# Kernel tuning notes

Measured on AMD Instinct MI355X. Metric: run time of the kernel, lower is better.

The kernel has to match this reference:

```python
import jax, jax.numpy as jnp
import numpy as np

INPUT_DIM = 1024
OUTPUT_DIM = 1024
DEGREE = 8


def setup_inputs() -> dict:
    key = jax.random.key(0)
    k1, k2 = jax.random.split(key)
    x = jax.random.normal(k1, (8192, INPUT_DIM), dtype=jnp.float32)
    std = 1.0 / (INPUT_DIM * (DEGREE + 1))
    cheby_coeffs = jax.random.normal(k2, (INPUT_DIM, OUTPUT_DIM, DEGREE + 1), dtype=jnp.float32) * std
    return {"x": x, "cheby_coeffs": cheby_coeffs}


def reference(x, cheby_coeffs):
    # x: [B, I]; cheby_coeffs: [I, O, D+1]
    degree = cheby_coeffs.shape[-1] - 1
    t = jnp.clip(jnp.tanh(x), -0.999, 0.999)            # [B, I]
    theta = jnp.arccos(t)[..., None]                     # [B, I, 1]
    arange = jnp.arange(degree + 1, dtype=x.dtype)       # [D+1]
    basis = jnp.cos(theta * arange)                      # [B, I, D+1] Chebyshev T_d(t)
    y = jnp.einsum('bid,iod->bo', basis, cheby_coeffs)   # [B, O]
    return y
```

## Files before the change

### kernel.cpp

```cpp
#include <hip/hip_runtime.h>
#include <stdint.h>

#define B_ROWS 8192
#define I_DIM  1024
#define N_DIM  1024
#define NDEG   9
#define K_DIM  (I_DIM * (NDEG-1))

#define BM 256
#define BN 128
#define BK 64
#define NT (K_DIM / BK)

typedef __attribute__((ext_vector_type(8)))  short short8;
typedef __attribute__((ext_vector_type(16))) float f32x16;

__device__ __forceinline__ unsigned short f2bf(float f) {
  union { float f; uint32_t u; } v; v.f = f;
  uint32_t u = v.u;
  u += 0x7FFFu + ((u >> 16) & 1u);
  return (unsigned short)(u >> 16);
}

__device__ __forceinline__ float bf2f(unsigned short h) {
  union { uint32_t u; float f; } v; v.u = ((uint32_t)h) << 16;
  return v.f;
}

__device__ __forceinline__ uint32_t pk_bf16(float lo, float hi) {
  uint32_t r;
  asm("v_cvt_pk_bf16_f32 %0, %1, %2" : "=v"(r) : "v"(lo), "v"(hi));
  return r;
}

__device__ __forceinline__ float fast_tanh(float x) {
  float e = __expf(2.0f * x);
  return 1.0f - __fdividef(2.0f, e + 1.0f);
}

__device__ __forceinline__ int h2(int r) { return (r >> 2) & 7; }

__global__ __launch_bounds__(256) void repack_kernel(const float* __restrict__ cf,
                                                     unsigned short* __restrict__ Bt,
                                                     float* __restrict__ bias) {
  __shared__ unsigned short L[32][584];
  const int i0  = blockIdx.x * 32;
  const int o0  = blockIdx.y * 64;
  const int tid = threadIdx.x;

  #pragma unroll
  for (int j = 0; j < 18; ++j) {
    const int f4  = j * 256 + tid;
    const int il  = f4 / 144;
    const int odq = f4 % 144;
    const float4 v = *reinterpret_cast<const float4*>(
        cf + ((size_t)(i0 + il) * N_DIM + o0) * NDEG + (size_t)odq * 4);
    ushort4 w;
    w.x = f2bf(v.x); w.y = f2bf(v.y); w.z = f2bf(v.z); w.w = f2bf(v.w);
    *reinterpret_cast<ushort4*>(&L[il][odq * 4]) = w;
  }
  __syncthreads();

  const int o  = tid >> 2;
  const int ci = tid & 3;
  const size_t base = (size_t)(o0 + o) * K_DIM + (size_t)(i0 + ci * 8) * 8;
  #pragma unroll
  for (int p = 0; p < 8; ++p) {
    const int il = ci * 8 + p;
    uint4 u;
    u.x = (uint32_t)L[il][o*9 + 1] | ((uint32_t)L[il][o*9 + 2] << 16);
    u.y = (uint32_t)L[il][o*9 + 3] | ((uint32_t)L[il][o*9 + 4] << 16);
    u.z = (uint32_t)L[il][o*9 + 5] | ((uint32_t)L[il][o*9 + 6] << 16);
    u.w = (uint32_t)L[il][o*9 + 7] | ((uint32_t)L[il][o*9 + 8] << 16);
    *reinterpret_cast<uint4*>(Bt + base + (size_t)p * 8) = u;
  }
  if (tid < 64) {
    float s = 0.f;
    #pragma unroll
    for (int il = 0; il < 32; ++il) s += bf2f(L[il][tid * 9]);
    atomicAdd(&bias[o0 + tid], s);
  }
}

__global__ __launch_bounds__(512, 2) void gemm_kernel(const float* __restrict__ x,
                                                      const unsigned short* __restrict__ Bt,
                                                      const float* __restrict__ bias,
                                                      float* __restrict__ C) {
  extern __shared__ unsigned short sm[];
  const int tid  = threadIdx.x;
  const int lane = tid & 63;
  const int wave = tid >> 6;
  const int l31  = lane & 31;
  const int half = lane >> 5;
  const int wm   = wave >> 1;
  const int wn   = wave & 1;

  const int bid = blockIdx.x;
  const int mt  = (bid & 7) + 8 * (bid >> 6);
  const int nt  = (bid >> 3) & 7;
  const int m0  = mt * BM;
  const int n0  = nt * BN;

  const int sr   = tid >> 3;
  const int slot = tid & 7;

  const unsigned short* Bbase = Bt + (size_t)n0 * K_DIM;

  int awoff[4];
  const float* xptr[4];
  #pragma unroll
  for (int q = 0; q < 4; ++q) {
    const int r_ = q * 64 + sr;
    awoff[q] = r_ * 64 + (slot ^ h2(r_)) * 8;
    xptr[q]  = x + (size_t)(m0 + r_) * I_DIM + slot;
  }

  f32x16 acc[2][2];
  #pragma unroll
  for (int a = 0; a < 2; ++a)
    #pragma unroll
    for (int b = 0; b < 2; ++b)
      #pragma unroll
      for (int r = 0; r < 16; ++r)
        acc[a][b][r] = 0.f;

#define STAGE_B(s, bf, kk) { const int r_ = (s)*64 + sr; const int gc_ = slot ^ h2(r_);     \
    __builtin_amdgcn_global_load_lds(                                                       \
        (const __attribute__((address_space(1))) void*)(Bbase + (size_t)r_*K_DIM + (kk) + gc_*8), \
        (__attribute__((address_space(3))) void*)&sm[32768 + (bf)*8192 + r_*64 + slot*8], 16, 0, 0); }

#define LOADX(xr, tt) {                                                                     \
    _Pragma("unroll")                                                                       \
    for (int q = 0; q < 4; ++q) xr[q] = xptr[q][(tt) * 8]; }

#define BASIS_Q(bf, q, xv) {                                                                \
      float t = fast_tanh(xv);                                                              \
      t = fminf(fmaxf(t, -0.999f), 0.999f);                                                 \
      const float t2 = t + t;                                                               \
      const float T1 = t;                                                                   \
      const float T2 = t2*t - 1.0f;                                                         \
      const float T3 = t2*T2 - T1;                                                          \
      const float T4 = t2*T3 - T2;                                                          \
      const float T5 = t2*T4 - T3;                                                          \
      const float T6 = t2*T5 - T4;                                                          \
      const float T7 = t2*T6 - T5;                                                          \
      const float T8 = t2*T7 - T6;                                                          \
      uint4 u;                                                                              \
      u.x = pk_bf16(T1, T2); u.y = pk_bf16(T3, T4);                                         \
      u.z = pk_bf16(T5, T6); u.w = pk_bf16(T7, T8);                                         \
      *reinterpret_cast<uint4*>(&sm[(bf)*16384 + awoff[q]]) = u; }

  const int rowA0 = wm * 64 + l31;
  const int rowA1 = wm * 64 + 32 + l31;
  const int rowB0 = wn * 64 + l31;
  const int rowB1 = wn * 64 + 32 + l31;
  const int hA0 = h2(rowA0), hA1 = h2(rowA1), hB0 = h2(rowB0), hB1 = h2(rowB1);

#define READ4(Asc, Bsc, av, bv, ks) {                                                        \
    const int c_ = (ks) * 2 + half;                                                          \
    av[0][ks] = *reinterpret_cast<const short8*>(&Asc[rowA0 * 64 + (c_ ^ hA0) * 8]);         \
    av[1][ks] = *reinterpret_cast<const short8*>(&Asc[rowA1 * 64 + (c_ ^ hA1) * 8]);         \
    bv[0][ks] = *reinterpret_cast<const short8*>(&Bsc[rowB0 * 64 + (c_ ^ hB0) * 8]);         \
    bv[1][ks] = *reinterpret_cast<const short8*>(&Bsc[rowB1 * 64 + (c_ ^ hB1) * 8]); }

#define MFMA4(av, bv, ks)                                                                    \
    acc[0][0] = __builtin_amdgcn_mfma_f32_32x32x16_bf16(av[0][ks], bv[0][ks], acc[0][0], 0, 0, 0); \
    acc[0][1] = __builtin_amdgcn_mfma_f32_32x32x16_bf16(av[0][ks], bv[1][ks], acc[0][1], 0, 0, 0); \
    acc[1][0] = __builtin_amdgcn_mfma_f32_32x32x16_bf16(av[1][ks], bv[0][ks], acc[1][0], 0, 0, 0); \
    acc[1][1] = __builtin_amdgcn_mfma_f32_32x32x16_bf16(av[1][ks], bv[1][ks], acc[1][1], 0, 0, 0);

#define TILE_FULL(kt_, XC, XL, LOADEN) {                                                     \
    const int cur_ = (kt_) & 1; const int nxt_ = cur_ ^ 1;                                   \
    const unsigned short* Asc = &sm[cur_ * 16384];                                           \
    const unsigned short* Bsc = &sm[32768 + cur_ * 8192];                                    \
    STAGE_B(0, nxt_, ((kt_) + 1) * BK) STAGE_B(1, nxt_, ((kt_) + 1) * BK)                    \
    if (LOADEN) { LOADX(XL, (kt_) + 2) }                                                     \
    __builtin_amdgcn_sched_barrier(0);                                                       \
    short8 av[2][4], bv[2][4];                                                               \
    READ4(Asc, Bsc, av, bv, 0)                                                               \
    READ4(Asc, Bsc, av, bv, 1)                                                               \
    BASIS_Q(nxt_, 0, XC[0])                                                                  \
    MFMA4(av, bv, 0)                                                                         \
    __builtin_amdgcn_sched_group_barrier(0x100, 8, 0);                                       \
    __builtin_amdgcn_sched_group_barrier(0x200, 1, 0);                                       \
    __builtin_amdgcn_sched_group_barrier(0x008, 4, 0);                                       \
    READ4(Asc, Bsc, av, bv, 2)                                                               \
    BASIS_Q(nxt_, 1, XC[1])                                                                  \
    MFMA4(av, bv, 1)                                                                         \
    __builtin_amdgcn_sched_group_barrier(0x100, 4, 0);                                       \
    __builtin_amdgcn_sched_group_barrier(0x200, 1, 0);                                       \
    __builtin_amdgcn_sched_group_barrier(0x008, 4, 0);                                       \
    READ4(Asc, Bsc, av, bv, 3)                                                               \
    BASIS_Q(nxt_, 2, XC[2])                                                                  \
    MFMA4(av, bv, 2)                                                                         \
    __builtin_amdgcn_sched_group_barrier(0x100, 4, 0);                                       \
    __builtin_amdgcn_sched_group_barrier(0x200, 1, 0);                                       \
    __builtin_amdgcn_sched_group_barrier(0x008, 4, 0);                                       \
    BASIS_Q(nxt_, 3, XC[3])                                                                  \
    MFMA4(av, bv, 3)                                                                         \
    __builtin_amdgcn_sched_group_barrier(0x200, 1, 0);                                       \
    __builtin_amdgcn_sched_group_barrier(0x008, 4, 0);                                       \
    __builtin_amdgcn_sched_barrier(0);                                                       \
    if (LOADEN) asm volatile("s_waitcnt vmcnt(4) lgkmcnt(0)" ::: "memory");                  \
    else        asm volatile("s_waitcnt vmcnt(0) lgkmcnt(0)" ::: "memory");                  \
    __builtin_amdgcn_s_barrier();                                                            \
    __builtin_amdgcn_sched_barrier(0); }

  float xrA[4], xrB[4];
  STAGE_B(0, 0, 0) STAGE_B(1, 0, 0)
  LOADX(xrA, 0)
  LOADX(xrB, 1)
  asm volatile("s_waitcnt vmcnt(4)" ::: "memory");
  BASIS_Q(0, 0, xrA[0]) BASIS_Q(0, 1, xrA[1]) BASIS_Q(0, 2, xrA[2]) BASIS_Q(0, 3, xrA[3])
  asm volatile("s_waitcnt lgkmcnt(0)" ::: "memory");
  __builtin_amdgcn_s_barrier();
  __builtin_amdgcn_sched_barrier(0);

  for (int kt = 0; kt < 126; kt += 2) {
    TILE_FULL(kt,     xrB, xrA, 1)
    TILE_FULL(kt + 1, xrA, xrB, 1)
  }
  TILE_FULL(126, xrB, xrA, 0)

  {
    const unsigned short* Asc = &sm[1 * 16384];
    const unsigned short* Bsc = &sm[32768 + 1 * 8192];
    short8 av[2][4], bv[2][4];
    READ4(Asc, Bsc, av, bv, 0)
    #pragma unroll
    for (int ks = 0; ks < 4; ++ks) {
      if (ks < 3) READ4(Asc, Bsc, av, bv, ks + 1)
      MFMA4(av, bv, ks)
      if (ks < 3) __builtin_amdgcn_sched_group_barrier(0x100, 4, 0);
      __builtin_amdgcn_sched_group_barrier(0x008, 4, 0);
    }
  }
#undef TILE_FULL
#undef MFMA4
#undef READ4
#undef BASIS_Q
#undef LOADX
#undef STAGE_B

  #pragma unroll
  for (int ni = 0; ni < 2; ++ni) {
    const int col  = n0 + wn * 64 + ni * 32 + l31;
    const float bc = bias[col];
    #pragma unroll
    for (int mi = 0; mi < 2; ++mi) {
      const int rbase = m0 + wm * 64 + mi * 32 + 4 * half;
      #pragma unroll
      for (int r = 0; r < 16; ++r) {
        const int row = rbase + (r & 3) + 8 * (r >> 2);
        C[(size_t)row * N_DIM + col] = acc[mi][ni][r] + bc;
      }
    }
  }
}

extern "C" void kernel_launch(void* const* d_in, const int* in_sizes, int n_in,
                              void* d_out, int out_size, void* d_ws, size_t ws_size,
                              hipStream_t stream) {
  const float* x      = (const float*)d_in[0];
  const float* coeffs = (const float*)d_in[1];
  float* y            = (float*)d_out;

  const size_t bt_bytes = (size_t)N_DIM * K_DIM * sizeof(unsigned short);
  unsigned short* Bt = (unsigned short*)d_ws;
  float* bias        = (float*)((char*)d_ws + bt_bytes);

  hipMemsetAsync(bias, 0, N_DIM * sizeof(float), stream);

  hipFuncSetAttribute((const void*)gemm_kernel,
                      hipFuncAttributeMaxDynamicSharedMemorySize, 98304);

  repack_kernel<<<dim3(I_DIM / 32, N_DIM / 64), 256, 0, stream>>>(coeffs, Bt, bias);
  gemm_kernel<<<(B_ROWS / BM) * (N_DIM / BN), 512, 98304, stream>>>(x, Bt, bias, y);
}
```

Measured before the change: 256.0 us.

## Triple-buffer LDS and double-buffer fragment registers in fused Chebyshev GEMM

Switches the GEMM main loop from two LDS buffers to three, so B tiles are staged two iterations ahead and the basis for tile k+2 is computed while tile k is consumed. Shared-memory fragments for the next k-tile are read into a second register set during the current MFMAs, which hides LDS read latency across the barrier. LDS per block grows to 144KB and register pressure rises from the doubled fragment arrays, which may limit occupancy or cause spills.

Result: slower. 274.9 us (+7.4%).

```diff
diff --git a/kernel.cpp b/kernel.cpp
--- a/kernel.cpp
+++ b/kernel.cpp
@@ -124,10 +124,14 @@
       for (int r = 0; r < 16; ++r)
         acc[a][b][r] = 0.f;
 
-#define STAGE_B(s, bf, kk) { const int r_ = (s)*64 + sr; const int gc_ = slot ^ h2(r_);     \
-    __builtin_amdgcn_global_load_lds(                                                       \
+#define STAGE_B2(bf, kk) {                                                                  \
+    _Pragma("unroll")                                                                       \
+    for (int s_ = 0; s_ < 2; ++s_) {                                                        \
+      const int r_ = s_ * 64 + sr; const int gc_ = slot ^ h2(r_);                           \
+      __builtin_amdgcn_global_load_lds(                                                     \
         (const __attribute__((address_space(1))) void*)(Bbase + (size_t)r_*K_DIM + (kk) + gc_*8), \
-        (__attribute__((address_space(3))) void*)&sm[32768 + (bf)*8192 + r_*64 + slot*8], 16, 0, 0); }
+        (__attribute__((address_space(3))) void*)&sm[49152 + (bf)*8192 + r_*64 + slot*8], 16, 0, 0); \
+    } }
 
 #define LOADX(xr, tt) {                                                                     \
     _Pragma("unroll")                                                                       \
@@ -156,12 +160,12 @@
   const int rowB1 = wn * 64 + 32 + l31;
   const int hA0 = h2(rowA0), hA1 = h2(rowA1), hB0 = h2(rowB0), hB1 = h2(rowB1);
 
-#define READ4(Asc, Bsc, av, bv, ks) {                                                        \
+#define READ4(Ar, Br, av, bv, ks) {                                                          \
     const int c_ = (ks) * 2 + half;                                                          \
-    av[0][ks] = *reinterpret_cast<const short8*>(&Asc[rowA0 * 64 + (c_ ^ hA0) * 8]);         \
-    av[1][ks] = *reinterpret_cast<const short8*>(&Asc[rowA1 * 64 + (c_ ^ hA1) * 8]);         \
-    bv[0][ks] = *reinterpret_cast<const short8*>(&Bsc[rowB0 * 64 + (c_ ^ hB0) * 8]);         \
-    bv[1][ks] = *reinterpret_cast<const short8*>(&Bsc[rowB1 * 64 + (c_ ^ hB1) * 8]); }
+    av[0][ks] = *reinterpret_cast<const short8*>(&(Ar)[rowA0 * 64 + (c_ ^ hA0) * 8]);        \
+    av[1][ks] = *reinterpret_cast<const short8*>(&(Ar)[rowA1 * 64 + (c_ ^ hA1) * 8]);        \
+    bv[0][ks] = *reinterpret_cast<const short8*>(&(Br)[rowB0 * 64 + (c_ ^ hB0) * 8]);        \
+    bv[1][ks] = *reinterpret_cast<const short8*>(&(Br)[rowB1 * 64 + (c_ ^ hB1) * 8]); }
 
 #define MFMA4(av, bv, ks)                                                                    \
     acc[0][0] = __builtin_amdgcn_mfma_f32_32x32x16_bf16(av[0][ks], bv[0][ks], acc[0][0], 0, 0, 0); \
@@ -169,78 +173,70 @@
     acc[1][0] = __builtin_amdgcn_mfma_f32_32x32x16_bf16(av[1][ks], bv[0][ks], acc[1][0], 0, 0, 0); \
     acc[1][1] = __builtin_amdgcn_mfma_f32_32x32x16_bf16(av[1][ks], bv[1][ks], acc[1][1], 0, 0, 0);
 
-#define TILE_FULL(kt_, XC, XL, LOADEN) {                                                     \
-    const int cur_ = (kt_) & 1; const int nxt_ = cur_ ^ 1;                                   \
-    const unsigned short* Asc = &sm[cur_ * 16384];                                           \
-    const unsigned short* Bsc = &sm[32768 + cur_ * 8192];                                    \
-    STAGE_B(0, nxt_, ((kt_) + 1) * BK) STAGE_B(1, nxt_, ((kt_) + 1) * BK)                    \
-    if (LOADEN) { LOADX(XL, (kt_) + 2) }                                                     \
+#define KS_STEP(AVc, BVc, AVr, BVr, XC, c2_, Ar_, Br_, ks, DO_RD, DO_PREP)                   \
+    if (DO_RD) { READ4(Ar_, Br_, AVr, BVr, ks) }                                            \
+    if (DO_PREP) { BASIS_Q((c2_), ks, (XC)[ks]) }                                           \
+    MFMA4(AVc, BVc, ks)                                                                      \
+    if (DO_RD)   __builtin_amdgcn_sched_group_barrier(0x100, 4, 0);                          \
+    if (DO_PREP) __builtin_amdgcn_sched_group_barrier(0x200, 1, 0);                          \
+    __builtin_amdgcn_sched_group_barrier(0x008, 4, 0);
+
+#define TILE(kt_, AVc, BVc, AVr, BVr, XC, XL, c1_, c2_, DO_RD, DO_PREP, DO_LX, DO_BAR) {     \
+    if (DO_PREP) { STAGE_B2((c2_), ((kt_) + 2) * BK) }                                       \
     __builtin_amdgcn_sched_barrier(0);                                                       \
-    short8 av[2][4], bv[2][4];                                                               \
-    READ4(Asc, Bsc, av, bv, 0)                                                               \
-    READ4(Asc, Bsc, av, bv, 1)                                                               \
-    BASIS_Q(nxt_, 0, XC[0])                                                                  \
-    MFMA4(av, bv, 0)                                                                         \
-    __builtin_amdgcn_sched_group_barrier(0x100, 8, 0);                                       \
-    __builtin_amdgcn_sched_group_barrier(0x200, 1, 0);                                       \
-    __builtin_amdgcn_sched_group_barrier(0x008, 4, 0);                                       \
-    READ4(Asc, Bsc, av, bv, 2)                                                               \
-    BASIS_Q(nxt_, 1, XC[1])                                                                  \
-    MFMA4(av, bv, 1)                                                                         \
-    __builtin_amdgcn_sched_group_barrier(0x100, 4, 0);                                       \
-    __builtin_amdgcn_sched_group_barrier(0x200, 1, 0);                                       \
-    __builtin_amdgcn_sched_group_barrier(0x008, 4, 0);                                       \
-    READ4(Asc, Bsc, av, bv, 3)                                                               \
-    BASIS_Q(nxt_, 2, XC[2])                                                                  \
-    MFMA4(av, bv, 2)                                                                         \
-    __builtin_amdgcn_sched_group_barrier(0x100, 4, 0);                                       \
-    __builtin_amdgcn_sched_group_barrier(0x200, 1, 0);                                       \
-    __builtin_amdgcn_sched_group_barrier(0x008, 4, 0);                                       \
-    BASIS_Q(nxt_, 3, XC[3])                                                                  \
-    MFMA4(av, bv, 3)                                                                         \
-    __builtin_amdgcn_sched_group_barrier(0x200, 1, 0);                                       \
-    __builtin_amdgcn_sched_group_barrier(0x008, 4, 0);                                       \
+    const unsigned short* Ar_ = &sm[(c1_) * 16384];                                          \
+    const unsigned short* Br_ = &sm[49152 + (c1_) * 8192];                                   \
+    KS_STEP(AVc, BVc, AVr, BVr, XC, c2_, Ar_, Br_, 0, DO_RD, DO_PREP)                        \
+    KS_STEP(AVc, BVc, AVr, BVr, XC, c2_, Ar_, Br_, 1, DO_RD, DO_PREP)                        \
+    KS_STEP(AVc, BVc, AVr, BVr, XC, c2_, Ar_, Br_, 2, DO_RD, DO_PREP)                        \
+    KS_STEP(AVc, BVc, AVr, BVr, XC, c2_, Ar_, Br_, 3, DO_RD, DO_PREP)                        \
     __builtin_amdgcn_sched_barrier(0);                                                       \
-    if (LOADEN) asm volatile("s_waitcnt vmcnt(4) lgkmcnt(0)" ::: "memory");                  \
-    else        asm volatile("s_waitcnt vmcnt(0) lgkmcnt(0)" ::: "memory");                  \
-    __builtin_amdgcn_s_barrier();                                                            \
-    __builtin_amdgcn_sched_barrier(0); }
+    if (DO_LX) { LOADX(XL, (kt_) + 4) }                                                      \
+    if (DO_BAR) {                                                                            \
+      if (DO_LX) { asm volatile("s_waitcnt vmcnt(4) lgkmcnt(0)" ::: "memory"); }             \
+      else       { asm volatile("s_waitcnt vmcnt(0) lgkmcnt(0)" ::: "memory"); }             \
+      __builtin_amdgcn_s_barrier();                                                          \
+      __builtin_amdgcn_sched_barrier(0);                                                     \
+    } }
 
   float xrA[4], xrB[4];
-  STAGE_B(0, 0, 0) STAGE_B(1, 0, 0)
+  short8 avA[2][4], bvA[2][4], avB[2][4], bvB[2][4];
   LOADX(xrA, 0)
   LOADX(xrB, 1)
-  asm volatile("s_waitcnt vmcnt(4)" ::: "memory");
+  STAGE_B2(0, 0)
+  STAGE_B2(1, BK)
+  asm volatile("s_waitcnt vmcnt(8)" ::: "memory");
   BASIS_Q(0, 0, xrA[0]) BASIS_Q(0, 1, xrA[1]) BASIS_Q(0, 2, xrA[2]) BASIS_Q(0, 3, xrA[3])
-  asm volatile("s_waitcnt lgkmcnt(0)" ::: "memory");
+  LOADX(xrA, 2)
+  asm volatile("s_waitcnt vmcnt(8)" ::: "memory");
+  BASIS_Q(1, 0, xrB[0]) BASIS_Q(1, 1, xrB[1]) BASIS_Q(1, 2, xrB[2]) BASIS_Q(1, 3, xrB[3])
+  LOADX(xrB, 3)
+  asm volatile("s_waitcnt vmcnt(8) lgkmcnt(0)" ::: "memory");
   __builtin_amdgcn_s_barrier();
-  __builtin_amdgcn_sched_barrier(0);
-
-  for (int kt = 0; kt < 126; kt += 2) {
-    TILE_FULL(kt,     xrB, xrA, 1)
-    TILE_FULL(kt + 1, xrA, xrB, 1)
-  }
-  TILE_FULL(126, xrB, xrA, 0)
-
   {
-    const unsigned short* Asc = &sm[1 * 16384];
-    const unsigned short* Bsc = &sm[32768 + 1 * 8192];
-    short8 av[2][4], bv[2][4];
-    READ4(Asc, Bsc, av, bv, 0)
-    #pragma unroll
-    for (int ks = 0; ks < 4; ++ks) {
-      if (ks < 3) READ4(Asc, Bsc, av, bv, ks + 1)
-      MFMA4(av, bv, ks)
-      if (ks < 3) __builtin_amdgcn_sched_group_barrier(0x100, 4, 0);
-      __builtin_amdgcn_sched_group_barrier(0x008, 4, 0);
-    }
-  }
-#undef TILE_FULL
+    const unsigned short* Ar_ = &sm[0];
+    const unsigned short* Br_ = &sm[49152];
+    READ4(Ar_, Br_, avA, bvA, 0) READ4(Ar_, Br_, avA, bvA, 1)
+    READ4(Ar_, Br_, avA, bvA, 2) READ4(Ar_, Br_, avA, bvA, 3)
+  }
+
+  int r0 = 0, r1 = 1, r2 = 2;
+  for (int kt = 0; kt < 124; kt += 2) {
+    TILE(kt,     avA, bvA, avB, bvB, xrA, xrA, r1, r2, 1, 1, 1, 1)
+    TILE(kt + 1, avB, bvB, avA, bvA, xrB, xrB, r2, r0, 1, 1, 1, 1)
+    const int t_ = r0; r0 = r2; r2 = r1; r1 = t_;
+  }
+  TILE(124, avA, bvA, avB, bvB, xrA, xrA, 2, 0, 1, 1, 0, 1)
+  TILE(125, avB, bvB, avA, bvA, xrB, xrB, 0, 1, 1, 1, 0, 1)
+  TILE(126, avA, bvA, avB, bvB, xrA, xrA, 1, 2, 1, 0, 0, 1)
+  TILE(127, avB, bvB, avA, bvA, xrB, xrB, 2, 0, 0, 0, 0, 0)
+#undef TILE
+#undef KS_STEP
 #undef MFMA4
 #undef READ4
 #undef BASIS_Q
 #undef LOADX
-#undef STAGE_B
+#undef STAGE_B2
 
   #pragma unroll
   for (int ni = 0; ni < 2; ++ni) {
@@ -272,8 +268,8 @@
   hipMemsetAsync(bias, 0, N_DIM * sizeof(float), stream);
 
   hipFuncSetAttribute((const void*)gemm_kernel,
-                      hipFuncAttributeMaxDynamicSharedMemorySize, 98304);
+                      hipFuncAttributeMaxDynamicSharedMemorySize, 147456);
 
   repack_kernel<<<dim3(I_DIM / 32, N_DIM / 64), 256, 0, stream>>>(coeffs, Bt, bias);
-  gemm_kernel<<<(B_ROWS / BM) * (N_DIM / BN), 512, 98304, stream>>>(x, Bt, bias, y);
-}
+  gemm_kernel<<<(B_ROWS / BM) * (N_DIM / BN), 512, 147456, stream>>>(x, Bt, bias, y);
+}
```
